# Kernel tuning notes

Hardware: AMD Instinct MI355X
Metric: run time of the kernel (lower is better)

The kernel has to match this reference:

```python
import jax, jax.numpy as jnp
import numpy as np

B, T, HID = 4, 4096, 768
H, D = 12, 64
N_HASHES = 2
BUCKET_SIZE = T // 32          # reformer repo config: max_seq_len // 32 = 128
N_BUCKETS = T // BUCKET_SIZE   # 32
SELF_ATTN_VALUE = -5e4         # reformer_pytorch TOKEN_SELF_ATTN_VALUE
MASK_VALUE = -1e9


def lsh_attention(X, mask_bool, W_qk, W_v, rotations):
    # X: [b, t, hid]; rotations: [d, n_hashes, n_buckets//2] (shared across batch & heads)
    b, t, _ = X.shape
    d, n_hashes, half_nb = rotations.shape
    n_buckets = 2 * half_nb
    h = W_qk.shape[0] // d
    scale = d ** -0.5

    qk = X @ W_qk.T            # shared query/key projection (bias-free in reformer_pytorch)
    v = X @ W_v.T

    def merge_heads(x):  # [b,t,h*d] -> [b*h, t, d]
        return x.reshape(b, t, h, d).transpose(0, 2, 1, 3).reshape(b * h, t, d)

    qk, v = merge_heads(qk), merge_heads(v)
    maskbh = jnp.repeat(mask_bool, h, axis=0)          # [bh, t]

    # --- LSH bucketing ---
    rotated = jnp.einsum('btf,fhi->bhti', qk, rotations)          # [bh, nh, t, nb/2]
    rotated = jnp.concatenate([rotated, -rotated], axis=-1)       # [bh, nh, t, nb]
    buckets = jnp.argmax(rotated, axis=-1)                        # [bh, nh, t]
    offsets = (jnp.arange(n_hashes) * n_buckets)[None, :, None]
    buckets = (buckets + offsets).reshape(b * h, n_hashes * t)

    # --- stable sort by (bucket, position) ---
    total = n_hashes * t
    ticker = jnp.arange(total)[None, :]
    buckets_and_t = buckets * t + (ticker % t)
    sticker = jnp.argsort(buckets_and_t, axis=-1)   # stable
    undo = jnp.argsort(sticker, axis=-1)
    st = sticker % t                                 # original positions, sorted order

    sqk = jnp.take_along_axis(qk, st[..., None], axis=1)
    sv = jnp.take_along_axis(v, st[..., None], axis=1)
    smask = jnp.take_along_axis(maskbh, st, axis=1)

    # --- chunk; each chunk attends to itself + previous chunk ---
    n_chunks = n_hashes * n_buckets
    cl = total // n_chunks                                  # == bucket_size
    bq_t = st.reshape(b * h, n_chunks, cl)
    bqk = sqk.reshape(b * h, n_chunks, cl, d)
    bv = sv.reshape(b * h, n_chunks, cl, d)
    bmask = smask.reshape(b * h, n_chunks, cl)

    bq = bqk
    bk = bqk / jnp.clip(jnp.linalg.norm(bqk, axis=-1, keepdims=True), 1e-12)

    def look_one_back(x):
        return jnp.concatenate([x, jnp.roll(x, 1, axis=1)], axis=2)

    bk, bv = look_one_back(bk), look_one_back(bv)
    bkv_t = look_one_back(bq_t)
    bkv_mask = look_one_back(bmask)

    dots = jnp.einsum('bnie,bnje->bnij', bq, bk) * scale    # [bh, n_chunks, cl, 2cl]
    pad = bmask[..., :, None] & bkv_mask[..., None, :]
    dots = jnp.where(pad, dots, MASK_VALUE)
    self_mask = bq_t[..., :, None] == bkv_t[..., None, :]
    dots = jnp.where(self_mask, SELF_ATTN_VALUE, dots)

    lse = jax.scipy.special.logsumexp(dots, axis=-1, keepdims=True)
    probs = jnp.exp(dots - lse)
    bo = jnp.einsum('bnij,bnje->bnie', probs, bv)

    # --- unsort and combine hash rounds via softmax over round logsumexps ---
    so = bo.reshape(b * h, total, d)
    slogits = lse.reshape(b * h, total)
    o = jnp.take_along_axis(so, undo[..., None], axis=1)
    logits = jnp.take_along_axis(slogits, undo, axis=1)

    o = o.reshape(b * h, n_hashes, t, d)
    logits = logits.reshape(b * h, n_hashes, t, 1)
    round_probs = jnp.exp(logits - jax.scipy.special.logsumexp(logits, axis=1, keepdims=True))
    out = jnp.sum(o * round_probs, axis=1)                  # [bh, t, d]
    return out.reshape(b, h, t, d).transpose(0, 2, 1, 3).reshape(b, t, h * d)


def setup_inputs() -> dict:
    key = jax.random.key(0)
    ks = jax.random.split(key, 8)
    s = 1.0 / np.sqrt(HID)
    return {
        'X': jax.random.normal(ks[0], (B, T, HID), jnp.float32),
        'mask': jnp.ones((B, T), jnp.float32),
        'W_qk': jax.random.uniform(ks[1], (H * D, HID), jnp.float32, -s, s),
        'W_v': jax.random.uniform(ks[2], (H * D, HID), jnp.float32, -s, s),
        'rotations': jax.random.normal(ks[3], (D, N_HASHES, N_BUCKETS // 2), jnp.float32),
        'W_to': jax.random.uniform(ks[4], (HID, H * D), jnp.float32, -s, s),
        'b_to': jnp.zeros((HID,), jnp.float32),
        'W_o': jax.random.uniform(ks[5], (HID, HID), jnp.float32, -s, s),
        'b_o': jnp.zeros((HID,), jnp.float32),
    }


def reference(X, mask, W_qk, W_v, rotations, W_to, b_to, W_o, b_o):
    attn = lsh_attention(X, mask.astype(bool), W_qk, W_v, rotations)
    attn = attn @ W_to.T + b_to     # LSHSelfAttention.to_out
    return attn @ W_o.T + b_o       # ReformerAttention.W_o
```

## Files before the change

kernel.cpp:

```cpp
#include <hip/hip_runtime.h>
#include <hip/hip_bf16.h>
#include <math.h>


typedef __attribute__((ext_vector_type(8))) short bf16x8;
typedef __attribute__((ext_vector_type(4))) float f32x4;
typedef __attribute__((ext_vector_type(4))) double f64x4;

__device__ __forceinline__ float bf_lo(unsigned int w) { return __uint_as_float(w << 16); }
__device__ __forceinline__ float bf_hi(unsigned int w) { return __uint_as_float(w & 0xffff0000u); }
__device__ __forceinline__ float load_in(const void* p, size_t i, bool f32) {
  return f32 ? ((const float*)p)[i]
             : __bfloat162float(((const __hip_bfloat16*)p)[i]);
}
__device__ __forceinline__ unsigned short f2bf(float x) {
  __hip_bfloat16 h = __float2bfloat16(x);
  return *reinterpret_cast<unsigned short*>(&h);
}
__device__ __forceinline__ float bf2f(unsigned short u) { return __uint_as_float(((unsigned int)u) << 16); }

__global__ void k_detect(const unsigned int* __restrict__ X, int* __restrict__ flag) {
  if (threadIdx.x == 0 && blockIdx.x == 0) {
    int vote = 0;
    for (int i = 0; i < 64; ++i) {
      unsigned int e = (X[i] >> 7) & 0xffu;
      vote += (e >= 100u && e <= 141u) ? 1 : 0;
    }
    *flag = (vote < 32) ? 1 : 0;
  }
}

__global__ __launch_bounds__(256) void k_convert(
    const void* __restrict__ src, unsigned short* __restrict__ dst, int n,
    const int* __restrict__ flag) {
  const bool f32in = (*flag != 0);
  int i = blockIdx.x * 256 + threadIdx.x;
  if (i >= n) return;
  if (f32in) dst[i] = f2bf(((const float*)src)[i]);
  else       dst[i] = ((const unsigned short*)src)[i];
}

__global__ __launch_bounds__(256) void k_build_wrot(
    const void* __restrict__ Wqk, const void* __restrict__ rot,
    double* __restrict__ WrotT, const int* __restrict__ flag) {
  const bool f32in = (*flag != 0);
  int idx = blockIdx.x * 256 + threadIdx.x;
  if (idx >= 768 * 384) return;
  int row = idx % 384;
  int c   = idx / 384;
  int hh = row >> 5, hi = row & 31;
  double s = 0.0;
  for (int f = 0; f < 64; ++f) {
    double rv = (double)load_in(rot, f * 32 + hi, f32in);
    double wv = (double)load_in(Wqk, (size_t)(hh * 64 + f) * 768 + c, f32in);
    s = fma(rv, wv, s);
  }
  WrotT[(size_t)c * 384 + row] = s;
}

__global__ __launch_bounds__(256) void k_bucket(
    const void* __restrict__ X, const double* __restrict__ WrotT,
    unsigned char* __restrict__ cls, const int* __restrict__ flag) {
  const bool f32in = (*flag != 0);
  __shared__ double SH[6336];
  double* Xs = SH;
  double* Ws = SH + 2080;
  double* Sc = SH;
  const int tid = threadIdx.x;
  const int M0 = blockIdx.x * 128;
  const int N0 = blockIdx.y * 96;
  const int w = tid >> 6, lane = tid & 63;
  const int l15 = lane & 15, lq = lane >> 4;
  const int sr = tid >> 1, sh = tid & 1;
  const int wk = tid >> 4, wg = tid & 15;

  f64x4 acc[2][6];
  #pragma unroll
  for (int i = 0; i < 2; ++i)
    #pragma unroll
    for (int j = 0; j < 6; ++j) acc[i][j] = (f64x4){0.0, 0.0, 0.0, 0.0};

  int rowid[4], colid[4];
  {
    f64x4 zz = (f64x4){0.0, 0.0, 0.0, 0.0};
    f64x4 pr = __builtin_amdgcn_mfma_f64_16x16x4f64(
        (double)l15, (lq == 0) ? 1.0 : 0.0, zz, 0, 0, 0);
    f64x4 pc = __builtin_amdgcn_mfma_f64_16x16x4f64(
        (lq == 0) ? 1.0 : 0.0, (double)l15, zz, 0, 0, 0);
    #pragma unroll
    for (int r = 0; r < 4; ++r) {
      rowid[r] = (int)pr[r];
      colid[r] = (int)pc[r];
    }
  }

  double xv[8];
  double wvv[6];
  auto load_chunk = [&](int k0) {
    size_t base = (size_t)(M0 + sr) * 768 + k0 + sh * 8;
    if (f32in) {
      const float4* fp = (const float4*)((const float*)X + base);
      float4 f0 = fp[0], f1 = fp[1];
      xv[0] = f0.x; xv[1] = f0.y; xv[2] = f0.z; xv[3] = f0.w;
      xv[4] = f1.x; xv[5] = f1.y; xv[6] = f1.z; xv[7] = f1.w;
    } else {
      uint4 u = *(const uint4*)((const unsigned short*)X + base);
      xv[0] = (double)bf_lo(u.x); xv[1] = (double)bf_hi(u.x);
      xv[2] = (double)bf_lo(u.y); xv[3] = (double)bf_hi(u.y);
      xv[4] = (double)bf_lo(u.z); xv[5] = (double)bf_hi(u.z);
      xv[6] = (double)bf_lo(u.w); xv[7] = (double)bf_hi(u.w);
    }
    const double* wp = WrotT + (size_t)(k0 + wk) * 384 + N0 + wg * 6;
    #pragma unroll
    for (int e = 0; e < 6; ++e) wvv[e] = wp[e];
  };

  load_chunk(0);
  for (int k0 = 0; k0 < 768; k0 += 16) {
    __syncthreads();
    #pragma unroll
    for (int j = 0; j < 8; ++j) Xs[(sh * 8 + j) * 130 + sr] = xv[j];
    #pragma unroll
    for (int e = 0; e < 6; ++e) Ws[wk * 98 + wg * 6 + e] = wvv[e];
    __syncthreads();
    if (k0 < 752) load_chunk(k0 + 16);
    #pragma unroll
    for (int kq = 0; kq < 4; ++kq) {
      const double* xr = &Xs[(kq * 4 + lq) * 130 + l15];
      double a0 = xr[w * 32];
      double a1 = xr[w * 32 + 16];
      const double* wr = &Ws[(kq * 4 + lq) * 98 + l15];
      #pragma unroll
      for (int nt = 0; nt < 6; ++nt) {
        double b = wr[nt * 16];
        acc[0][nt] = __builtin_amdgcn_mfma_f64_16x16x4f64(a0, b, acc[0][nt], 0, 0, 0);
        acc[1][nt] = __builtin_amdgcn_mfma_f64_16x16x4f64(a1, b, acc[1][nt], 0, 0, 0);
      }
    }
  }

  #pragma unroll
  for (int chunk = 0; chunk < 2; ++chunk) {
    __syncthreads();
    if ((w >> 1) == chunk) {
      int lr = (w & 1) * 32;
      #pragma unroll
      for (int mt = 0; mt < 2; ++mt)
        #pragma unroll
        for (int nt = 0; nt < 6; ++nt)
          #pragma unroll
          for (int r = 0; r < 4; ++r)
            Sc[(nt * 16 + colid[r]) * 66 + lr + mt * 16 + rowid[r]] = acc[mt][nt][r];
    }
    __syncthreads();
    for (int task = tid; task < 384; task += 256) {
      int g = task >> 6, tok = task & 63;
      const double* s = &Sc[(g * 16) * 66 + tok];
      double mx = -1.0e300;
      #pragma unroll
      for (int i = 0; i < 16; ++i) {
        double a = s[i * 66];
        mx = fmax(mx, fmax(a, -a));
      }
      int amax = 0;
      #pragma unroll
      for (int i = 15; i >= 0; --i) if (-s[i * 66] == mx) amax = 16 + i;
      #pragma unroll
      for (int i = 15; i >= 0; --i) if (s[i * 66] == mx) amax = i;
      int m = M0 + chunk * 64 + tok;
      int b = m >> 12, t = m & 4095;
      int gg = blockIdx.y * 6 + g, hh = gg >> 1, h = gg & 1;
      cls[(size_t)(b * 12 + hh) * 8192 + h * 4096 + t] = (unsigned char)(h * 32 + amax);
    }
  }
}

__global__ __launch_bounds__(1024) void k_sort(
    const unsigned char* __restrict__ clsg,
    unsigned short* __restrict__ stick) {
  __shared__ unsigned short cntg[128 * 64];
  __shared__ int classbase[64];
  const int row = blockIdx.x;
  const int tid = threadIdx.x;
  const int wave = tid >> 6, lane = tid & 63;
  const unsigned char* cr = clsg + ((size_t)row << 13);

  for (int i = tid; i < 128 * 64 / 2; i += 1024) ((uint32_t*)cntg)[i] = 0;
  __syncthreads();

  unsigned char myc[8], myrank[8];
  const unsigned long long ltmask = (lane == 0) ? 0ull : (~0ull >> (64 - lane));
  #pragma unroll
  for (int chunk = 0; chunk < 8; ++chunk) {
    int g = chunk * 16 + wave;
    int j = g * 64 + lane;
    int c = cr[j];
    unsigned long long same = ~0ull;
    #pragma unroll
    for (int bit = 0; bit < 6; ++bit) {
      unsigned long long bm = __ballot((c >> bit) & 1);
      same &= ((c >> bit) & 1) ? bm : ~bm;
    }
    int rank = __popcll(same & ltmask);
    if (rank == 0) cntg[g * 64 + c] = (unsigned short)__popcll(same);
    myc[chunk] = (unsigned char)c;
    myrank[chunk] = (unsigned char)rank;
  }
  __syncthreads();
  if (tid < 64) {
    int run = 0;
    for (int g = 0; g < 128; ++g) {
      int t = cntg[g * 64 + tid];
      cntg[g * 64 + tid] = (unsigned short)run;
      run += t;
    }
    classbase[tid] = run;
  }
  __syncthreads();
  if (tid == 0) {
    int run = 0;
    for (int c = 0; c < 64; ++c) { int t = classbase[c]; classbase[c] = run; run += t; }
  }
  __syncthreads();
  unsigned short* out = stick + ((size_t)row << 13);
  #pragma unroll
  for (int chunk = 0; chunk < 8; ++chunk) {
    int g = chunk * 16 + wave;
    int j = g * 64 + lane;
    int c = myc[chunk];
    int pos = classbase[c] + cntg[g * 64 + c] + myrank[chunk];
    out[pos] = (unsigned short)j;
  }
}

__global__ __launch_bounds__(256) void k_gemm_mfma(
    const unsigned short* __restrict__ A, const unsigned short* __restrict__ W,
    const void* __restrict__ bias, void* __restrict__ Cout,
    int layout, int out_ext, const int* __restrict__ flag) {
  const bool f32in = (*flag != 0);
  const bool oF32 = out_ext && f32in;
  __shared__ unsigned short As[128 * 40];
  __shared__ unsigned short Bs[128 * 40];
  const int tid = threadIdx.x;
  const int bm = blockIdx.x, bn = blockIdx.y;
  const int w = tid >> 6, lane = tid & 63;
  const int l15 = lane & 15, lq = lane >> 4;
  const int wm = (w >> 1) * 64, wn = (w & 1) * 64;
  const int r4 = tid >> 2, c4 = tid & 3;
  const unsigned short* Ag = A + (size_t)(bm * 128 + r4) * 768 + c4 * 8;
  const unsigned short* Bg = W + (size_t)(bn * 128 + r4) * 768 + c4 * 8;
  f32x4 acc[4][4];
  #pragma unroll
  for (int i = 0; i < 4; ++i)
    #pragma unroll
    for (int j = 0; j < 4; ++j) acc[i][j] = (f32x4){0.f, 0.f, 0.f, 0.f};
  uint4 pa0 = *(const uint4*)(Ag);
  uint4 pa1 = *(const uint4*)(Ag + 64 * 768);
  uint4 pb0 = *(const uint4*)(Bg);
  uint4 pb1 = *(const uint4*)(Bg + 64 * 768);
  for (int kt = 0; kt < 24; ++kt) {
    __syncthreads();
    *(uint4*)&As[r4 * 40 + c4 * 8] = pa0;
    *(uint4*)&As[(r4 + 64) * 40 + c4 * 8] = pa1;
    *(uint4*)&Bs[r4 * 40 + c4 * 8] = pb0;
    *(uint4*)&Bs[(r4 + 64) * 40 + c4 * 8] = pb1;
    __syncthreads();
    if (kt < 23) {
      int off = (kt + 1) * 32;
      pa0 = *(const uint4*)(Ag + off);
      pa1 = *(const uint4*)(Ag + 64 * 768 + off);
      pb0 = *(const uint4*)(Bg + off);
      pb1 = *(const uint4*)(Bg + 64 * 768 + off);
    }
    bf16x8 af[4], bfr[4];
    #pragma unroll
    for (int mt = 0; mt < 4; ++mt)
      af[mt] = *(const bf16x8*)&As[(wm + mt * 16 + l15) * 40 + lq * 8];
    #pragma unroll
    for (int nt = 0; nt < 4; ++nt)
      bfr[nt] = *(const bf16x8*)&Bs[(wn + nt * 16 + l15) * 40 + lq * 8];
    #pragma unroll
    for (int mt = 0; mt < 4; ++mt)
      #pragma unroll
      for (int nt = 0; nt < 4; ++nt)
        acc[mt][nt] = __builtin_amdgcn_mfma_f32_16x16x32_bf16(af[mt], bfr[nt], acc[mt][nt], 0, 0, 0);
  }
  #pragma unroll
  for (int mt = 0; mt < 4; ++mt) {
    #pragma unroll
    for (int nt = 0; nt < 4; ++nt) {
      #pragma unroll
      for (int reg = 0; reg < 4; ++reg) {
        int m = bm * 128 + wm + mt * 16 + lq * 4 + reg;
        int n = bn * 128 + wn + nt * 16 + l15;
        float val = acc[mt][nt][reg];
        if (bias != nullptr) val += load_in(bias, n, f32in);
        if (layout == 0) {
          size_t addr = (size_t)m * 768 + n;
          if (oF32) ((float*)Cout)[addr] = val;
          else      ((unsigned short*)Cout)[addr] = f2bf(val);
        } else {
          int b2 = m >> 12, t2 = m & 4095, hh = n >> 6, f = n & 63;
          ((unsigned short*)Cout)[((((size_t)(b2 * 12 + hh)) << 12) + t2) * 64 + f] = f2bf(val);
        }
      }
    }
  }
}

__global__ __launch_bounds__(256) void k_norm(
    const unsigned short* __restrict__ qk, float* __restrict__ nk) {
  int row = blockIdx.x * 32 + (threadIdx.x >> 3);
  int cs = threadIdx.x & 7;
  const uint4* p = (const uint4*)(qk + (size_t)row * 64);
  uint4 wv = p[cs];
  float s = 0.f;
  float e;
  e = bf_lo(wv.x); s += e * e;  e = bf_hi(wv.x); s += e * e;
  e = bf_lo(wv.y); s += e * e;  e = bf_hi(wv.y); s += e * e;
  e = bf_lo(wv.z); s += e * e;  e = bf_hi(wv.z); s += e * e;
  e = bf_lo(wv.w); s += e * e;  e = bf_hi(wv.w); s += e * e;
  s += __shfl_xor(s, 1, 64);
  s += __shfl_xor(s, 2, 64);
  s += __shfl_xor(s, 4, 64);
  if (cs == 0) nk[row] = 1.0f / fmaxf(sqrtf(s), 1e-12f);
}

__global__ __launch_bounds__(256) void k_attn_mfma(
    const unsigned short* __restrict__ qk,
    const unsigned short* __restrict__ vv,
    const unsigned short* __restrict__ stick,
    const void* __restrict__ mask,
    const float* __restrict__ nk,
    unsigned short* __restrict__ o_r,
    float* __restrict__ lse_r,
    const int* __restrict__ flag) {
  const bool f32in = (*flag != 0);
  __shared__ unsigned short Qs[128 * 72];
  __shared__ unsigned short Ks[64 * 72];
  __shared__ unsigned short Vt[64 * 72];
  __shared__ unsigned short Ps[4 * 32 * 72];
  __shared__ unsigned short Tq[128];
  __shared__ unsigned short Tkv[64];
  __shared__ float Nkv[64];
  unsigned short* Vs = Ps;

  const int tid = threadIdx.x;
  const int bh = blockIdx.x >> 6;
  const int ci = blockIdx.x & 63;
  const int b  = bh / 12;
  const int prev = (ci + 63) & 63;
  const int w = tid >> 6, lane = tid & 63;
  const int l15 = lane & 15, lq = lane >> 4;
  const unsigned short* srow = stick + ((size_t)bh << 13);
  const int jrow = tid >> 3, cs = tid & 7;

  #pragma unroll
  for (int pass = 0; pass < 4; ++pass) {
    int r = jrow + pass * 32;
    int s = srow[ci * 128 + r];
    int t = s & 4095;
    uint4 qw = ((const uint4*)(qk + ((((size_t)bh << 12) + t) << 6)))[cs];
    *(uint4*)&Qs[r * 72 + cs * 8] = qw;
    if (cs == 0) {
      float mv = load_in(mask, b * 4096 + t, f32in);
      Tq[r] = (unsigned short)(s | ((mv != 0.0f) ? 0 : 0x8000));
    }
  }
  __syncthreads();

  unsigned short tqr[2][4];
  #pragma unroll
  for (int mt = 0; mt < 2; ++mt)
    #pragma unroll
    for (int reg = 0; reg < 4; ++reg)
      tqr[mt][reg] = Tq[w * 32 + mt * 16 + lq * 4 + reg];

  float m_run[2][4], l_run[2][4];
  f32x4 oacc[2][4];
  #pragma unroll
  for (int mt = 0; mt < 2; ++mt)
    #pragma unroll
    for (int reg = 0; reg < 4; ++reg) { m_run[mt][reg] = -3.0e38f; l_run[mt][reg] = 0.0f; }
  #pragma unroll
  for (int mt = 0; mt < 2; ++mt)
    #pragma unroll
    for (int nto = 0; nto < 4; ++nto) oacc[mt][nto] = (f32x4){0.f, 0.f, 0.f, 0.f};

  for (int kt = 0; kt < 4; ++kt) {
    __syncthreads();
    #pragma unroll
    for (int pass = 0; pass < 2; ++pass) {
      int j = jrow + pass * 32;
      int chunk = (kt < 2) ? ci : prev;
      int s = srow[chunk * 128 + (kt & 1) * 64 + j];
      int t = s & 4095;
      const uint4* kb = (const uint4*)(qk + ((((size_t)bh << 12) + t) << 6));
      *(uint4*)&Ks[j * 72 + cs * 8] = kb[cs];
      const uint4* vb = (const uint4*)(vv + ((((size_t)bh << 12) + t) << 6));
      int sw = (cs ^ (j & 7) ^ (j >> 3)) & 7;
      *(uint4*)&Vs[j * 72 + sw * 8] = vb[cs];
      if (cs == 0) {
        float mv = load_in(mask, b * 4096 + t, f32in);
        Tkv[j] = (unsigned short)(t | ((mv != 0.0f) ? 0 : 0x8000));
        Nkv[j] = nk[((size_t)bh << 12) + t] * 0.125f;
      }
    }
    __syncthreads();

    #pragma unroll
    for (int i = 0; i < 8; ++i) {
      int cp = w * 8 + i;
      int q8 = cp >> 2;
      int sw = (q8 ^ (lane & 7) ^ (lane >> 3)) & 7;
      uint32_t wv = *(const uint32_t*)&Vs[lane * 72 + sw * 8 + ((2 * cp) & 7)];
      Vt[(2 * cp) * 72 + lane]     = (unsigned short)(wv & 0xffff);
      Vt[(2 * cp + 1) * 72 + lane] = (unsigned short)(wv >> 16);
    }

    f32x4 sacc[2][4];
    #pragma unroll
    for (int mt = 0; mt < 2; ++mt)
      #pragma unroll
      for (int nt = 0; nt < 4; ++nt) sacc[mt][nt] = (f32x4){0.f, 0.f, 0.f, 0.f};
    #pragma unroll
    for (int ks = 0; ks < 2; ++ks) {
      bf16x8 af[2];
      #pragma unroll
      for (int mt = 0; mt < 2; ++mt)
        af[mt] = *(const bf16x8*)&Qs[(w * 32 + mt * 16 + l15) * 72 + ks * 32 + lq * 8];
      #pragma unroll
      for (int nt = 0; nt < 4; ++nt) {
        bf16x8 bfr = *(const bf16x8*)&Ks[(nt * 16 + l15) * 72 + ks * 32 + lq * 8];
        #pragma unroll
        for (int mt = 0; mt < 2; ++mt)
          sacc[mt][nt] = __builtin_amdgcn_mfma_f32_16x16x32_bf16(af[mt], bfr, sacc[mt][nt], 0, 0, 0);
      }
    }

    unsigned short tkc[4];
    float nkc[4];
    #pragma unroll
    for (int nt = 0; nt < 4; ++nt) {
      tkc[nt] = Tkv[nt * 16 + l15];
      nkc[nt] = Nkv[nt * 16 + l15];
    }
    float dv[2][4][4];
    #pragma unroll
    for (int mt = 0; mt < 2; ++mt)
      #pragma unroll
      for (int nt = 0; nt < 4; ++nt)
        #pragma unroll
        for (int reg = 0; reg < 4; ++reg) {
          float x = sacc[mt][nt][reg] * nkc[nt];
          unsigned short ts = tqr[mt][reg];
          if (((tkc[nt] | ts) & 0x8000) != 0) x = -1.0e9f;
          if (((tkc[nt] ^ ts) & 0x0fff) == 0) x = -5.0e4f;
          dv[mt][nt][reg] = x;
        }
    float mn[2][4], scv[2][4];
    #pragma unroll
    for (int mt = 0; mt < 2; ++mt)
      #pragma unroll
      for (int reg = 0; reg < 4; ++reg) {
        float rm = fmaxf(fmaxf(dv[mt][0][reg], dv[mt][1][reg]),
                         fmaxf(dv[mt][2][reg], dv[mt][3][reg]));
        rm = fmaxf(rm, __shfl_xor(rm, 1, 64));
        rm = fmaxf(rm, __shfl_xor(rm, 2, 64));
        rm = fmaxf(rm, __shfl_xor(rm, 4, 64));
        rm = fmaxf(rm, __shfl_xor(rm, 8, 64));
        float mnew = fmaxf(m_run[mt][reg], rm);
        scv[mt][reg] = __expf(m_run[mt][reg] - mnew);
        m_run[mt][reg] = mnew;
        mn[mt][reg] = mnew;
      }
    #pragma unroll
    for (int mt = 0; mt < 2; ++mt)
      #pragma unroll
      for (int nt = 0; nt < 4; ++nt)
        #pragma unroll
        for (int reg = 0; reg < 4; ++reg)
          dv[mt][nt][reg] = __expf(dv[mt][nt][reg] - mn[mt][reg]);
    #pragma unroll
    for (int mt = 0; mt < 2; ++mt)
      #pragma unroll
      for (int reg = 0; reg < 4; ++reg) {
        float rs = ((dv[mt][0][reg] + dv[mt][1][reg]) + (dv[mt][2][reg] + dv[mt][3][reg]));
        rs += __shfl_xor(rs, 1, 64);
        rs += __shfl_xor(rs, 2, 64);
        rs += __shfl_xor(rs, 4, 64);
        rs += __shfl_xor(rs, 8, 64);
        l_run[mt][reg] = l_run[mt][reg] * scv[mt][reg] + rs;
      }
    #pragma unroll
    for (int mt = 0; mt < 2; ++mt)
      #pragma unroll
      for (int nto = 0; nto < 4; ++nto)
        #pragma unroll
        for (int reg = 0; reg < 4; ++reg)
          oacc[mt][nto][reg] *= scv[mt][reg];

    __syncthreads();

    #pragma unroll
    for (int mt = 0; mt < 2; ++mt)
      #pragma unroll
      for (int nt = 0; nt < 4; ++nt)
        #pragma unroll
        for (int reg = 0; reg < 4; ++reg)
          Ps[w * 2304 + (mt * 16 + lq * 4 + reg) * 72 + nt * 16 + l15] = f2bf(dv[mt][nt][reg]);

    #pragma unroll
    for (int ks = 0; ks < 2; ++ks) {
      bf16x8 pf[2];
      #pragma unroll
      for (int mt = 0; mt < 2; ++mt)
        pf[mt] = *(const bf16x8*)&Ps[w * 2304 + (mt * 16 + l15) * 72 + ks * 32 + lq * 8];
      #pragma unroll
      for (int nto = 0; nto < 4; ++nto) {
        bf16x8 vf = *(const bf16x8*)&Vt[(nto * 16 + l15) * 72 + ks * 32 + lq * 8];
        #pragma unroll
        for (int mt = 0; mt < 2; ++mt)
          oacc[mt][nto] = __builtin_amdgcn_mfma_f32_16x16x32_bf16(pf[mt], vf, oacc[mt][nto], 0, 0, 0);
      }
    }
  }

  float invl[2][4];
  #pragma unroll
  for (int mt = 0; mt < 2; ++mt)
    #pragma unroll
    for (int reg = 0; reg < 4; ++reg) {
      float lr = l_run[mt][reg];
      invl[mt][reg] = 1.0f / lr;
      if (l15 == 0) {
        int Rr = w * 32 + mt * 16 + lq * 4 + reg;
        int s = Tq[Rr];
        int tq0 = s & 4095, rq0 = (s >> 12) & 1;
        lse_r[(((size_t)(bh * 2 + rq0)) << 12) + tq0] = m_run[mt][reg] + __logf(lr);
      }
    }
  #pragma unroll
  for (int mt = 0; mt < 2; ++mt)
    #pragma unroll
    for (int nto = 0; nto < 4; ++nto)
      #pragma unroll
      for (int reg = 0; reg < 4; ++reg)
        Ps[w * 2304 + (mt * 16 + lq * 4 + reg) * 72 + nto * 16 + l15] =
            f2bf(oacc[mt][nto][reg] * invl[mt][reg]);
  #pragma unroll
  for (int pass = 0; pass < 4; ++pass) {
    int rl = pass * 8 + (lane >> 3);
    int s = Tq[w * 32 + rl];
    int tq0 = s & 4095, rq0 = (s >> 12) & 1;
    uint4 ov = *(const uint4*)&Ps[w * 2304 + rl * 72 + (lane & 7) * 8];
    *(uint4*)(o_r + ((((size_t)(bh * 2 + rq0)) << 12) + tq0) * 64 + (lane & 7) * 8) = ov;
  }
}

__global__ __launch_bounds__(256) void k_combine(
    const unsigned short* __restrict__ o_r,
    const float* __restrict__ lse_r,
    unsigned short* __restrict__ attn) {
  int idx = blockIdx.x * 256 + threadIdx.x;
  if (idx >= 48 * 4096 * 64) return;
  int f = idx & 63;
  int t = (idx >> 6) & 4095;
  int bh = idx >> 18;
  float l0 = lse_r[((size_t)(bh * 2 + 0) << 12) + t];
  float l1 = lse_r[((size_t)(bh * 2 + 1) << 12) + t];
  float mm = fmaxf(l0, l1);
  float e0 = __expf(l0 - mm), e1 = __expf(l1 - mm);
  float inv = 1.0f / (e0 + e1);
  float o0 = bf2f(o_r[(((size_t)(bh * 2 + 0) << 12) + t) * 64 + f]);
  float o1 = bf2f(o_r[(((size_t)(bh * 2 + 1) << 12) + t) * 64 + f]);
  float res = (e0 * o0 + e1 * o1) * inv;
  int b = bh / 12, hh = bh % 12;
  attn[((size_t)(b * 4096 + t)) * 768 + hh * 64 + f] = f2bf(res);
}

extern "C" void kernel_launch(void* const* d_in, const int* in_sizes, int n_in,
                              void* d_out, int out_size, void* d_ws, size_t ws_size,
                              hipStream_t stream) {
  (void)in_sizes; (void)n_in; (void)out_size; (void)ws_size;
  const void* X    = d_in[0];
  const void* mask = d_in[1];
  const void* Wqk  = d_in[2];
  const void* Wv   = d_in[3];
  const void* rot  = d_in[4];
  const void* Wto  = d_in[5];
  const void* bto  = d_in[6];
  const void* Wo   = d_in[7];
  const void* bo   = d_in[8];

  char* ws = (char*)d_ws;
  int*            flag  = (int*)(ws);
  unsigned short* stick = (unsigned short*)(ws + 256);
  float*          lse_r = (float*)(ws + 786688);
  float*          nk    = (float*)(ws + 2359552);
  unsigned short* qk    = (unsigned short*)(ws + 3145984);
  unsigned short* v     = (unsigned short*)(ws + 28311808);
  unsigned short* o_r   = (unsigned short*)(ws + 53477632);
  double*         WrotT = (double*)(ws + 53477632);
  unsigned char*  cls   = (unsigned char*)(ws + 55836928);
  unsigned short* Wqkb  = (unsigned short*)(ws + 56230144);
  unsigned short* Wvb   = (unsigned short*)(ws + 57409792);
  unsigned short* Xb    = (unsigned short*)(ws + 58589440);
  unsigned short* Wtob  = (unsigned short*)(ws + 53477632);
  unsigned short* Wob   = (unsigned short*)(ws + 54657280);
  unsigned short* attn  = v;
  unsigned short* tmp   = qk;

  k_detect<<<1, 64, 0, stream>>>((const unsigned int*)X, flag);
  k_convert<<<49152, 256, 0, stream>>>(X, Xb, 12582912, flag);
  k_convert<<<2304, 256, 0, stream>>>(Wqk, Wqkb, 589824, flag);
  k_convert<<<2304, 256, 0, stream>>>(Wv, Wvb, 589824, flag);
  k_build_wrot<<<1152, 256, 0, stream>>>(Wqk, rot, WrotT, flag);
  k_bucket<<<dim3(128, 4), 256, 0, stream>>>(X, WrotT, cls, flag);
  k_sort<<<48, 1024, 0, stream>>>(cls, stick);
  k_gemm_mfma<<<dim3(128, 6), 256, 0, stream>>>(Xb, Wqkb, nullptr, qk, 1, 0, flag);
  k_gemm_mfma<<<dim3(128, 6), 256, 0, stream>>>(Xb, Wvb,  nullptr, v,  1, 0, flag);
  k_norm<<<6144, 256, 0, stream>>>(qk, nk);
  k_attn_mfma<<<3072, 256, 0, stream>>>(qk, v, stick, mask, nk, o_r, lse_r, flag);
  k_combine<<<49152, 256, 0, stream>>>(o_r, lse_r, attn);
  k_convert<<<2304, 256, 0, stream>>>(Wto, Wtob, 589824, flag);
  k_convert<<<2304, 256, 0, stream>>>(Wo, Wob, 589824, flag);
  k_gemm_mfma<<<dim3(128, 6), 256, 0, stream>>>(attn, Wtob, bto, tmp, 0, 0, flag);
  k_gemm_mfma<<<dim3(128, 6), 256, 0, stream>>>(tmp, Wob, bo, d_out, 0, 1, flag);
}
```

Before: 658.4 us.

## Double-buffer k_bucket LDS tiles and widen block to 512 threads

```diff
diff --git a/kernel.cpp b/kernel.cpp
--- a/kernel.cpp
+++ b/kernel.cpp
@@ -58,27 +58,23 @@
   WrotT[(size_t)c * 384 + row] = s;
 }
 
-__global__ __launch_bounds__(256) void k_bucket(
+__global__ __launch_bounds__(512) void k_bucket(
     const void* __restrict__ X, const double* __restrict__ WrotT,
     unsigned char* __restrict__ cls, const int* __restrict__ flag) {
   const bool f32in = (*flag != 0);
-  __shared__ double SH[6336];
-  double* Xs = SH;
-  double* Ws = SH + 2080;
+  __shared__ double SH[7296];
   double* Sc = SH;
   const int tid = threadIdx.x;
   const int M0 = blockIdx.x * 128;
   const int N0 = blockIdx.y * 96;
   const int w = tid >> 6, lane = tid & 63;
   const int l15 = lane & 15, lq = lane >> 4;
-  const int sr = tid >> 1, sh = tid & 1;
-  const int wk = tid >> 4, wg = tid & 15;
-
-  f64x4 acc[2][6];
-  #pragma unroll
-  for (int i = 0; i < 2; ++i)
-    #pragma unroll
-    for (int j = 0; j < 6; ++j) acc[i][j] = (f64x4){0.0, 0.0, 0.0, 0.0};
+  const int sr = tid >> 2, sh2 = tid & 3;
+  const int wk = tid >> 5, wn3 = (tid & 31) * 3;
+
+  f64x4 acc[6];
+  #pragma unroll
+  for (int j = 0; j < 6; ++j) acc[j] = (f64x4){0.0, 0.0, 0.0, 0.0};
 
   int rowid[4], colid[4];
   {
@@ -94,66 +90,62 @@
     }
   }
 
-  double xv[8];
-  double wvv[6];
+  double xv[4];
+  double wvv[3];
   auto load_chunk = [&](int k0) {
-    size_t base = (size_t)(M0 + sr) * 768 + k0 + sh * 8;
+    size_t base = (size_t)(M0 + sr) * 768 + k0 + sh2 * 4;
     if (f32in) {
-      const float4* fp = (const float4*)((const float*)X + base);
-      float4 f0 = fp[0], f1 = fp[1];
+      float4 f0 = *(const float4*)((const float*)X + base);
       xv[0] = f0.x; xv[1] = f0.y; xv[2] = f0.z; xv[3] = f0.w;
-      xv[4] = f1.x; xv[5] = f1.y; xv[6] = f1.z; xv[7] = f1.w;
     } else {
-      uint4 u = *(const uint4*)((const unsigned short*)X + base);
+      uint2 u = *(const uint2*)((const unsigned short*)X + base);
       xv[0] = (double)bf_lo(u.x); xv[1] = (double)bf_hi(u.x);
       xv[2] = (double)bf_lo(u.y); xv[3] = (double)bf_hi(u.y);
-      xv[4] = (double)bf_lo(u.z); xv[5] = (double)bf_hi(u.z);
-      xv[6] = (double)bf_lo(u.w); xv[7] = (double)bf_hi(u.w);
-    }
-    const double* wp = WrotT + (size_t)(k0 + wk) * 384 + N0 + wg * 6;
-    #pragma unroll
-    for (int e = 0; e < 6; ++e) wvv[e] = wp[e];
+    }
+    const double* wp = WrotT + (size_t)(k0 + wk) * 384 + N0 + wn3;
+    wvv[0] = wp[0]; wvv[1] = wp[1]; wvv[2] = wp[2];
   };
+  auto store_stage = [&](int bsel) {
+    double* Xs = SH + bsel * 2080;
+    double* Ws = SH + 4160 + bsel * 1568;
+    #pragma unroll
+    for (int j = 0; j < 4; ++j) Xs[(sh2 * 4 + j) * 130 + sr] = xv[j];
+    #pragma unroll
+    for (int e = 0; e < 3; ++e) Ws[wk * 98 + wn3 + e] = wvv[e];
+  };
 
   load_chunk(0);
-  for (int k0 = 0; k0 < 768; k0 += 16) {
-    __syncthreads();
-    #pragma unroll
-    for (int j = 0; j < 8; ++j) Xs[(sh * 8 + j) * 130 + sr] = xv[j];
-    #pragma unroll
-    for (int e = 0; e < 6; ++e) Ws[wk * 98 + wg * 6 + e] = wvv[e];
-    __syncthreads();
-    if (k0 < 752) load_chunk(k0 + 16);
+  store_stage(0);
+  __syncthreads();
+  for (int t = 0; t < 48; ++t) {
+    const double* Xs = SH + (t & 1) * 2080;
+    const double* Ws = SH + 4160 + (t & 1) * 1568;
+    if (t < 47) load_chunk((t + 1) * 16);
     #pragma unroll
     for (int kq = 0; kq < 4; ++kq) {
-      const double* xr = &Xs[(kq * 4 + lq) * 130 + l15];
-      double a0 = xr[w * 32];
-      double a1 = xr[w * 32 + 16];
+      double a = Xs[(kq * 4 + lq) * 130 + w * 16 + l15];
       const double* wr = &Ws[(kq * 4 + lq) * 98 + l15];
       #pragma unroll
-      for (int nt = 0; nt < 6; ++nt) {
-        double b = wr[nt * 16];
-        acc[0][nt] = __builtin_amdgcn_mfma_f64_16x16x4f64(a0, b, acc[0][nt], 0, 0, 0);
-        acc[1][nt] = __builtin_amdgcn_mfma_f64_16x16x4f64(a1, b, acc[1][nt], 0, 0, 0);
-      }
-    }
+      for (int nt = 0; nt < 6; ++nt)
+        acc[nt] = __builtin_amdgcn_mfma_f64_16x16x4f64(a, wr[nt * 16], acc[nt], 0, 0, 0);
+    }
+    if (t < 47) store_stage((t & 1) ^ 1);
+    __syncthreads();
   }
 
   #pragma unroll
   for (int chunk = 0; chunk < 2; ++chunk) {
     __syncthreads();
-    if ((w >> 1) == chunk) {
-      int lr = (w & 1) * 32;
-      #pragma unroll
-      for (int mt = 0; mt < 2; ++mt)
+    if ((w >> 2) == chunk) {
+      int lr = (w & 3) * 16;
+      #pragma unroll
+      for (int nt = 0; nt < 6; ++nt)
         #pragma unroll
-        for (int nt = 0; nt < 6; ++nt)
-          #pragma unroll
-          for (int r = 0; r < 4; ++r)
-            Sc[(nt * 16 + colid[r]) * 66 + lr + mt * 16 + rowid[r]] = acc[mt][nt][r];
-    }
-    __syncthreads();
-    for (int task = tid; task < 384; task += 256) {
+        for (int r = 0; r < 4; ++r)
+          Sc[(nt * 16 + colid[r]) * 66 + lr + rowid[r]] = acc[nt][r];
+    }
+    __syncthreads();
+    for (int task = tid; task < 384; task += 512) {
       int g = task >> 6, tok = task & 63;
       const double* s = &Sc[(g * 16) * 66 + tok];
       double mx = -1.0e300;
@@ -616,7 +608,7 @@
   k_convert<<<2304, 256, 0, stream>>>(Wqk, Wqkb, 589824, flag);
   k_convert<<<2304, 256, 0, stream>>>(Wv, Wvb, 589824, flag);
   k_build_wrot<<<1152, 256, 0, stream>>>(Wqk, rot, WrotT, flag);
-  k_bucket<<<dim3(128, 4), 256, 0, stream>>>(X, WrotT, cls, flag);
+  k_bucket<<<dim3(128, 4), 512, 0, stream>>>(X, WrotT, cls, flag);
   k_sort<<<48, 1024, 0, stream>>>(cls, stick);
   k_gemm_mfma<<<dim3(128, 6), 256, 0, stream>>>(Xb, Wqkb, nullptr, qk, 1, 0, flag);
   k_gemm_mfma<<<dim3(128, 6), 256, 0, stream>>>(Xb, Wvb,  nullptr, v,  1, 0, flag);
```

Measured after the change: 645.0 us. 1.02x faster.
